# Kernel tuning notes

Hardware: AMD Instinct MI355X
Metric: run time of the kernel (lower is better)

## Reference

```python
import jax, jax.numpy as jnp
import numpy as np

NUM_HEADS = 16
NEG_INF = -9e15


def setup_inputs() -> dict:
    key = jax.random.key(0)
    k1, k2, k3 = jax.random.split(key, 3)
    B, S, D = 2, 2048, 1024
    # xavier-uniform-ish init scale for weights
    lim_qkv = float(np.sqrt(6.0 / (D + 3 * D)))
    lim_o = float(np.sqrt(6.0 / (D + D)))
    return {
        "x": jax.random.normal(k1, (B, S, D), dtype=jnp.float32),
        "w_qkv": jax.random.uniform(k2, (3 * D, D), minval=-lim_qkv, maxval=lim_qkv, dtype=jnp.float32),
        "b_qkv": jnp.zeros((3 * D,), dtype=jnp.float32),
        "w_o": jax.random.uniform(k3, (D, D), minval=-lim_o, maxval=lim_o, dtype=jnp.float32),
        "b_o": jnp.zeros((D,), dtype=jnp.float32),
    }


def reference(x, w_qkv, b_qkv, w_o, b_o):
    B, S, D = x.shape
    H = NUM_HEADS
    hd = D // H
    # qkv projection: [B,S,3D]
    qkv = x @ w_qkv.T + b_qkv
    # -> [B, H, S, 3*hd], then split
    qkv = qkv.reshape(B, S, H, 3 * hd).transpose(0, 2, 1, 3)
    q, k, v = jnp.split(qkv, 3, axis=-1)  # each [B,H,S,hd]
    scale = 1.0 / jnp.sqrt(jnp.asarray(hd, dtype=x.dtype))
    logits = jnp.einsum("bhqd,bhkd->bhqk", q, k) * scale
    attn = jax.nn.softmax(logits, axis=-1)
    vals = jnp.einsum("bhqk,bhkd->bhqd", attn, v)
    vals = vals.transpose(0, 2, 1, 3).reshape(B, S, D)
    return vals @ w_o.T + b_o
```

## Files before the change

kernel.cpp:

```cpp
#include <hip/hip_runtime.h>
#include <math.h>

#define NHEADS 16
#define HD 64

typedef __attribute__((ext_vector_type(8))) _Float16 half8;
typedef __attribute__((ext_vector_type(4))) _Float16 half4;
typedef __attribute__((ext_vector_type(4))) float f32x4;
typedef __attribute__((ext_vector_type(16))) float f32x16;
typedef __attribute__((ext_vector_type(4))) unsigned int u32x4;

__device__ inline void load_lds16(const void* g, void* l) {
    __builtin_amdgcn_global_load_lds(
        (const __attribute__((address_space(1))) unsigned int*)g,
        (__attribute__((address_space(3))) unsigned int*)l, 16, 0, 0);
}
__device__ inline void pl32swap(unsigned int& x, unsigned int& y) {
    asm volatile("v_permlane32_swap_b32 %0, %1" : "+v"(x), "+v"(y));
}

#define NX  4194304
#define NWQ 3145728
#define NWO 1048576
__global__ void cvt_all(const float* __restrict__ x, const float* __restrict__ wq,
                        const float* __restrict__ wo, _Float16* __restrict__ xf,
                        _Float16* __restrict__ wqf, _Float16* __restrict__ wof) {
    int i = (blockIdx.x * blockDim.x + threadIdx.x) * 8;
    const float* src; _Float16* dst; int off;
    if (i < NX)            { src = x;  dst = xf;  off = i; }
    else if (i < NX + NWQ) { src = wq; dst = wqf; off = i - NX; }
    else                   { src = wo; dst = wof; off = i - (NX + NWQ); }
    float4 a = *(const float4*)(src + off);
    float4 b = *(const float4*)(src + off + 4);
    half8 h;
    h[0] = (_Float16)a.x; h[1] = (_Float16)a.y; h[2] = (_Float16)a.z; h[3] = (_Float16)a.w;
    h[4] = (_Float16)b.x; h[5] = (_Float16)b.y; h[6] = (_Float16)b.z; h[7] = (_Float16)b.w;
    *(half8*)(dst + off) = h;
}

#define GEMM_SETUP(K, NTILE)                                                           \
    const int tid = threadIdx.x;                                                       \
    const int l = tid & 63, w = tid >> 6;                                              \
    const int wr = w >> 1, wc = w & 1;                                                 \
    const int nwg = gridDim.x * gridDim.y;                                             \
    const int bid = blockIdx.y * gridDim.x + blockIdx.x;                               \
    const int swz = (bid & 7) * (nwg >> 3) + (bid >> 3);                               \
    const int m0 = (swz / gridDim.x) * 128, n0 = (swz % gridDim.x) * (NTILE);          \
    const int srow = tid >> 2;                                                         \
    const int schunk = (tid & 3) ^ ((srow >> 1) & 3);                                  \
    const size_t gA0 = (size_t)(m0 + srow) * K + schunk * 8;                           \
    const size_t gA1 = gA0 + (size_t)64 * K;                                           \
    const size_t gB0 = (size_t)(n0 + srow) * K + schunk * 8;                           \
    unsigned char* ldsW = smem + w * 1024;                                             \
    const int col16 = l & 15, kc = l >> 4;                                             \
    const int ra0 = wr * 64 + col16;                                                   \
    const int offA = ra0 * 64 + ((kc ^ ((ra0 >> 1) & 3)) * 16);

#define QSCALE 0.18033688f
__global__ __launch_bounds__(256, 2) void gemm_qkv(
    const _Float16* __restrict__ A, const _Float16* __restrict__ B,
    const float* __restrict__ bias,
    _Float16* __restrict__ Qf, _Float16* __restrict__ Kf,
    _Float16* __restrict__ VfT, int K) {
    __shared__ __align__(1024) unsigned char smem[49152];
    GEMM_SETUP(K, 128)
    const size_t gB1 = gB0 + (size_t)64 * K;
    const int rb0 = wc * 64 + col16;
    const int offB = rb0 * 64 + ((kc ^ ((rb0 >> 1) & 3)) * 16);
    f32x4 acc[4][4] = {};

#define GSTAGE(k0_, buf_)                                                              \
    load_lds16(A + gA0 + (k0_), ldsW + (buf_) * 16384 + 0);                            \
    load_lds16(A + gA1 + (k0_), ldsW + (buf_) * 16384 + 4096);                         \
    load_lds16(B + gB0 + (k0_), ldsW + (buf_) * 16384 + 8192);                         \
    load_lds16(B + gB1 + (k0_), ldsW + (buf_) * 16384 + 12288);
#define GSTEP(s_, buf_, VM, dostage)                                                   \
    asm volatile("s_waitcnt " VM ::: "memory");                                        \
    __builtin_amdgcn_sched_barrier(0);                                                 \
    __builtin_amdgcn_s_barrier();                                                      \
    if (dostage) { GSTAGE(((s_) + 2) * 32, ((buf_) + 2) % 3) }                         \
    {                                                                                  \
        const unsigned char* bs = smem + (buf_) * 16384;                               \
        half8 af[4], bf[4];                                                            \
        _Pragma("unroll")                                                              \
        for (int m = 0; m < 4; ++m) af[m] = *(const half8*)(bs + offA + m * 1024);     \
        _Pragma("unroll")                                                              \
        for (int n = 0; n < 4; ++n) bf[n] = *(const half8*)(bs + 8192 + offB + n * 1024); \
        _Pragma("unroll")                                                              \
        for (int m = 0; m < 4; ++m)                                                    \
            _Pragma("unroll")                                                          \
            for (int n = 0; n < 4; ++n)                                                \
                acc[m][n] = __builtin_amdgcn_mfma_f32_16x16x32_f16(af[m], bf[n], acc[m][n], 0, 0, 0); \
    }

    GSTAGE(0, 0)
    GSTAGE(32, 1)
    for (int t = 0; t < 30; t += 3) {
        GSTEP(t, 0, "vmcnt(4)", 1)
        GSTEP(t + 1, 1, "vmcnt(4)", 1)
        GSTEP(t + 2, 2, "vmcnt(4)", 1)
    }
    GSTEP(30, 0, "vmcnt(4)", 0)
    GSTEP(31, 1, "vmcnt(0)", 0)
#undef GSTAGE
#undef GSTEP

    const int rowb = m0 + wr * 64 + (l >> 4) * 4;
    const int colb = n0 + wc * 64 + col16;
    #pragma unroll
    for (int n = 0; n < 4; ++n) {
        int col = colb + n * 16;
        int h = col / 192;
        int rem = col - h * 192;
        int part = rem >> 6, d = rem & 63;
        float bv = bias[col];
        #pragma unroll
        for (int m = 0; m < 4; ++m) {
            int r0 = rowb + m * 16;
            int b = r0 >> 11, s0r = r0 & 2047;
            int bh = b * 16 + h;
            if (part == 0) {
                #pragma unroll
                for (int j = 0; j < 4; ++j)
                    Qf[((size_t)bh * 2048 + s0r + j) * 64 + d] =
                        (_Float16)((acc[m][n][j] + bv) * QSCALE);
            } else if (part == 1) {
                #pragma unroll
                for (int j = 0; j < 4; ++j)
                    Kf[((size_t)bh * 2048 + s0r + j) * 64 + d] = (_Float16)(acc[m][n][j] + bv);
            } else {
                half4 pk;
                pk[0] = (_Float16)(acc[m][n][0] + bv);
                pk[1] = (_Float16)(acc[m][n][1] + bv);
                pk[2] = (_Float16)(acc[m][n][2] + bv);
                pk[3] = (_Float16)(acc[m][n][3] + bv);
                *(half4*)&VfT[((size_t)bh * 64 + d) * 2048 + s0r] = pk;
            }
        }
    }
}

__global__ __launch_bounds__(256, 2) void gemm_o(
    const _Float16* __restrict__ A, const _Float16* __restrict__ B,
    const float* __restrict__ bias, float* __restrict__ C,
    int M, int N, int K) {
    __shared__ __align__(1024) unsigned char smem[36864];
    GEMM_SETUP(K, 64)
    const int rb0 = wc * 32 + col16;
    const int offB = rb0 * 64 + ((kc ^ ((rb0 >> 1) & 3)) * 16);
    f32x4 acc[4][2] = {};

#define OSTAGE(k0_, buf_)                                                              \
    load_lds16(A + gA0 + (k0_), ldsW + (buf_) * 12288 + 0);                            \
    load_lds16(A + gA1 + (k0_), ldsW + (buf_) * 12288 + 4096);                         \
    load_lds16(B + gB0 + (k0_), ldsW + (buf_) * 12288 + 8192);
#define OSTEP(s_, buf_, VM, dostage)                                                   \
    asm volatile("s_waitcnt " VM ::: "memory");                                        \
    __builtin_amdgcn_sched_barrier(0);                                                 \
    __builtin_amdgcn_s_barrier();                                                      \
    if (dostage) { OSTAGE(((s_) + 2) * 32, ((buf_) + 2) % 3) }                         \
    {                                                                                  \
        const unsigned char* bs = smem + (buf_) * 12288;                               \
        half8 af[4], bf[2];                                                            \
        _Pragma("unroll")                                                              \
        for (int m = 0; m < 4; ++m) af[m] = *(const half8*)(bs + offA + m * 1024);     \
        _Pragma("unroll")                                                              \
        for (int n = 0; n < 2; ++n) bf[n] = *(const half8*)(bs + 8192 + offB + n * 1024); \
        _Pragma("unroll")                                                              \
        for (int m = 0; m < 4; ++m)                                                    \
            _Pragma("unroll")                                                          \
            for (int n = 0; n < 2; ++n)                                                \
                acc[m][n] = __builtin_amdgcn_mfma_f32_16x16x32_f16(af[m], bf[n], acc[m][n], 0, 0, 0); \
    }

    OSTAGE(0, 0)
    OSTAGE(32, 1)
    for (int t = 0; t < 30; t += 3) {
        OSTEP(t, 0, "vmcnt(3)", 1)
        OSTEP(t + 1, 1, "vmcnt(3)", 1)
        OSTEP(t + 2, 2, "vmcnt(3)", 1)
    }
    OSTEP(30, 0, "vmcnt(3)", 0)
    OSTEP(31, 1, "vmcnt(0)", 0)
#undef OSTAGE
#undef OSTEP

    const int rowb = m0 + wr * 64 + (l >> 4) * 4;
    const int colb = n0 + wc * 32 + col16;
    float bv[2];
    #pragma unroll
    for (int n = 0; n < 2; ++n) bv[n] = bias[colb + n * 16];
    #pragma unroll
    for (int m = 0; m < 4; ++m)
        #pragma unroll
        for (int j = 0; j < 4; ++j) {
            float* crow = C + (size_t)(rowb + m * 16 + j) * N + colb;
            #pragma unroll
            for (int n = 0; n < 2; ++n) crow[n * 16] = acc[m][n][j] + bv[n];
        }
}

__global__ __launch_bounds__(512, 2) void mfma_attn(
    const _Float16* __restrict__ Qf, const _Float16* __restrict__ Kf,
    const _Float16* __restrict__ VfT, _Float16* __restrict__ vals) {
    __shared__ __align__(1024) unsigned char smem[49152];
    const int tid = threadIdx.x;
    const int l = tid & 63, w = tid >> 6;
    const int l31 = l & 31, hl = l >> 5;
    const int hwbid = blockIdx.y * gridDim.x + blockIdx.x;
    const int q_t = (hwbid >> 3) & 7;
    const int bh = (hwbid & 7) + ((hwbid >> 6) << 3);
    const int q0 = q_t * 256;
    const int h = bh & 15, b = bh >> 4;

    half8 qf[4];
    {
        const _Float16* qp = Qf + ((size_t)bh * 2048 + q0 + w * 32 + l31) * 64 + hl * 8;
        #pragma unroll
        for (int c = 0; c < 4; ++c) qf[c] = *(const half8*)(qp + c * 16);
    }
    f32x16 zvec = {};
    f32x16 o0 = {}, o1 = {};
    float mshift = 0.f, lsum = 0.f;

    const _Float16* Kg = Kf + (size_t)bh * 2048 * 64;
    const _Float16* Vg = VfT + (size_t)bh * 64 * 2048;

    int offK, offV;
    {
        int row2 = w * 4 + (l >> 4);
        int slot = (l & 15) ^ (row2 & 15);
        int row = row2 * 2 + (slot >> 3);
        int chunk = slot & 7;
        offK = row * 64 + chunk * 8;
        offV = row * 2048 + chunk * 8;
    }
    const int sbase = (l31 & 1) * 8;
    const int xr = (l31 >> 1) & 15;
    const int rb0 = (l31 >> 1) * 256;

    #define STAGE(kt0, buf)                                                            \
        {                                                                              \
            unsigned char* bK = smem + (buf) * 8192 + w * 1024;                        \
            unsigned char* bV = smem + 24576 + (buf) * 8192 + w * 1024;                \
            load_lds16(Kg + (size_t)(kt0) * 64 + offK, bK);                            \
            load_lds16(Vg + (kt0) + offV, bV);                                         \
        }

    #define QK_TILE(kb, D0, D1)                                                        \
        {                                                                              \
            const unsigned char* Ksb_ = smem + (kb) * 8192;                            \
            {                                                                          \
                int chOff = ((sbase + hl) ^ xr) << 4;                                  \
                half8 k0_ = *(const half8*)(Ksb_ + rb0 + chOff);                       \
                half8 k1_ = *(const half8*)(Ksb_ + rb0 + 4096 + chOff);                \
                D0 = __builtin_amdgcn_mfma_f32_32x32x16_f16(k0_, qf[0], zvec, 0, 0, 0);\
                D1 = __builtin_amdgcn_mfma_f32_32x32x16_f16(k1_, qf[0], zvec, 0, 0, 0);\
            }                                                                          \
            _Pragma("unroll")                                                          \
            for (int kc = 1; kc < 4; ++kc) {                                           \
                int chOff = ((sbase + kc * 2 + hl) ^ xr) << 4;                         \
                half8 k0_ = *(const half8*)(Ksb_ + rb0 + chOff);                       \
                half8 k1_ = *(const half8*)(Ksb_ + rb0 + 4096 + chOff);                \
                D0 = __builtin_amdgcn_mfma_f32_32x32x16_f16(k0_, qf[kc], D0, 0, 0, 0); \
                D1 = __builtin_amdgcn_mfma_f32_32x32x16_f16(k1_, qf[kc], D1, 0, 0, 0); \
            }                                                                          \
        }

    #define SMPV(S0, S1, vb_)                                                          \
        {                                                                              \
            const unsigned char* Vsb_ = smem + 24576 + (vb_) * 8192;                   \
            if (__any(mshift != 0.f)) {                                                \
                _Pragma("unroll")                                                      \
                for (int r = 0; r < 16; ++r) { S0[r] -= mshift; S1[r] -= mshift; }     \
            }                                                                          \
            float r0 = 0.f, r1 = 0.f, r2 = 0.f, r3 = 0.f;                              \
            unsigned int a[2][8];                                                      \
            _Pragma("unroll")                                                          \
            for (int j = 0; j < 8; ++j) {                                              \
                float p0 = __builtin_amdgcn_exp2f(S0[2 * j]);                          \
                float p1 = __builtin_amdgcn_exp2f(S0[2 * j + 1]);                      \
                float q0_ = __builtin_amdgcn_exp2f(S1[2 * j]);                         \
                float q1_ = __builtin_amdgcn_exp2f(S1[2 * j + 1]);                     \
                r0 += p0; r1 += p1; r2 += q0_; r3 += q1_;                              \
                a[0][j] = __builtin_bit_cast(unsigned int, __builtin_amdgcn_cvt_pkrtz(p0, p1));   \
                a[1][j] = __builtin_bit_cast(unsigned int, __builtin_amdgcn_cvt_pkrtz(q0_, q1_)); \
            }                                                                          \
            float rsum = (r0 + r1) + (r2 + r3);                                        \
            if (__any(rsum > 32768.f)) {                                               \
                float pmax = S0[0];                                                    \
                _Pragma("unroll")                                                      \
                for (int r = 1; r < 16; ++r) pmax = fmaxf(pmax, S0[r]);                \
                _Pragma("unroll")                                                      \
                for (int r = 0; r < 16; ++r) pmax = fmaxf(pmax, S1[r]);                \
                pmax = fmaxf(pmax, __shfl_xor(pmax, 32, 64));                          \
                float d_ = fmaxf(pmax, 0.f);                                           \
                float corr = __builtin_amdgcn_exp2f(-d_);                              \
                _Pragma("unroll")                                                      \
                for (int r = 0; r < 16; ++r) { S0[r] -= d_; S1[r] -= d_; }             \
                _Pragma("unroll")                                                      \
                for (int r = 0; r < 16; ++r) { o0[r] *= corr; o1[r] *= corr; }         \
                lsum *= corr;                                                          \
                mshift += d_;                                                          \
                r0 = r1 = r2 = r3 = 0.f;                                               \
                _Pragma("unroll")                                                      \
                for (int j = 0; j < 8; ++j) {                                          \
                    float p0 = __builtin_amdgcn_exp2f(S0[2 * j]);                      \
                    float p1 = __builtin_amdgcn_exp2f(S0[2 * j + 1]);                  \
                    float q0_ = __builtin_amdgcn_exp2f(S1[2 * j]);                     \
                    float q1_ = __builtin_amdgcn_exp2f(S1[2 * j + 1]);                 \
                    r0 += p0; r1 += p1; r2 += q0_; r3 += q1_;                          \
                    a[0][j] = __builtin_bit_cast(unsigned int, __builtin_amdgcn_cvt_pkrtz(p0, p1));   \
                    a[1][j] = __builtin_bit_cast(unsigned int, __builtin_amdgcn_cvt_pkrtz(q0_, q1_)); \
                }                                                                      \
                rsum = (r0 + r1) + (r2 + r3);                                          \
            }                                                                          \
            lsum += rsum;                                                              \
            _Pragma("unroll")                                                          \
            for (int c = 0; c < 2; ++c) {                                              \
                pl32swap(a[c][0], a[c][2]);                                            \
                pl32swap(a[c][1], a[c][3]);                                            \
                pl32swap(a[c][4], a[c][6]);                                            \
                pl32swap(a[c][5], a[c][7]);                                            \
            }                                                                          \
            _Pragma("unroll")                                                          \
            for (int kk = 0; kk < 4; ++kk) {                                           \
                u32x4 pw;                                                              \
                pw.x = a[kk >> 1][(kk & 1) * 4 + 0];                                   \
                pw.y = a[kk >> 1][(kk & 1) * 4 + 1];                                   \
                pw.z = a[kk >> 1][(kk & 1) * 4 + 2];                                   \
                pw.w = a[kk >> 1][(kk & 1) * 4 + 3];                                   \
                half8 pf = __builtin_bit_cast(half8, pw);                              \
                int chOff = ((sbase + kk * 2 + hl) ^ xr) << 4;                         \
                half8 v0 = *(const half8*)(Vsb_ + rb0 + chOff);                        \
                half8 v1 = *(const half8*)(Vsb_ + rb0 + 4096 + chOff);                 \
                o0 = __builtin_amdgcn_mfma_f32_32x32x16_f16(v0, pf, o0, 0, 0, 0);      \
                o1 = __builtin_amdgcn_mfma_f32_32x32x16_f16(v1, pf, o1, 0, 0, 0);      \
            }                                                                          \
        }

    #define AITER(tt, kb, VM, dostage)                                                 \
        asm volatile("s_waitcnt " VM ::: "memory");                                    \
        __builtin_amdgcn_sched_barrier(0);                                             \
        __builtin_amdgcn_s_barrier();                                                  \
        if (dostage) STAGE(((tt) + 2) * 64, ((kb) + 2) % 3)                            \
        QK_TILE(kb, sS0, sS1)                                                          \
        SMPV(sS0, sS1, kb)

    STAGE(0, 0)
    STAGE(64, 1)
    f32x16 sS0, sS1;
    for (int t = 0; t < 30; t += 3) {
        AITER(t, 0, "vmcnt(2)", 1)
        AITER(t + 1, 1, "vmcnt(2)", 1)
        AITER(t + 2, 2, "vmcnt(2)", 1)
    }
    AITER(30, 0, "vmcnt(2)", 0)
    AITER(31, 1, "vmcnt(0)", 0)

    lsum += __shfl_xor(lsum, 32, 64);
    float inv = 1.f / lsum;
    size_t orow = ((size_t)(b * 2048 + q0 + w * 32 + l31)) * 1024 + h * 64;
    #pragma unroll
    for (int dc = 0; dc < 2; ++dc) {
        const f32x16* op = dc ? &o1 : &o0;
        #pragma unroll
        for (int rq = 0; rq < 4; ++rq) {
            int d0 = dc * 32 + rq * 8 + hl * 4;
            half4 hv;
            #pragma unroll
            for (int j = 0; j < 4; ++j) hv[j] = (_Float16)((*op)[rq * 4 + j] * inv);
            *(half4*)(vals + orow + d0) = hv;
        }
    }
}

extern "C" void kernel_launch(void* const* d_in, const int* in_sizes, int n_in,
                              void* d_out, int out_size, void* d_ws, size_t ws_size,
                              hipStream_t stream) {
    const float* x     = (const float*)d_in[0];
    const float* w_qkv = (const float*)d_in[1];
    const float* b_qkv = (const float*)d_in[2];
    const float* w_o   = (const float*)d_in[3];
    const float* b_o   = (const float*)d_in[4];
    float* out = (float*)d_out;

    const int B = 2, S = 2048, D = 1024;
    const int M = B * S;
    const int N1 = 3 * D;
    const int BH = B * NHEADS;

    _Float16* xf  = (_Float16*)d_ws;
    _Float16* wqf = xf  + (size_t)M * D;
    _Float16* wof = wqf + (size_t)N1 * D;
    _Float16* Qf  = wof + (size_t)D * D;
    _Float16* Kf  = Qf  + (size_t)BH * S * HD;
    _Float16* VfT = Kf  + (size_t)BH * S * HD;
    _Float16* vals = xf;

    cvt_all<<<(NX + NWQ + NWO) / 2048, 256, 0, stream>>>(x, w_qkv, w_o, xf, wqf, wof);

    gemm_qkv<<<dim3(N1 / 128, M / 128), 256, 0, stream>>>(xf, wqf, b_qkv, Qf, Kf, VfT, D);

    mfma_attn<<<dim3(S / 256, BH), 512, 0, stream>>>(Qf, Kf, VfT, vals);

    gemm_o<<<dim3(D / 64, M / 128), 256, 0, stream>>>(vals, wof, b_o, out, M, D, D);
}
```

Before: 107.2 us.

## Process KV tiles in pairs per barrier with doubled LDS ring

The attention loop now stages and consumes two 64-key K/V tiles per iteration. This halves the number of s_barrier/waitcnt synchronisation points and gives the scheduler two independent QK MFMA chains to interleave. LDS usage doubles to 96 KB per block, which with 512-thread blocks and launch_bounds(512,2) may reduce how many blocks fit per CU. It also raises register pressure from the extra score accumulators.

```diff
diff --git a/kernel.cpp b/kernel.cpp
--- a/kernel.cpp
+++ b/kernel.cpp
@@ -203,7 +203,7 @@
 __global__ __launch_bounds__(512, 2) void mfma_attn(
     const _Float16* __restrict__ Qf, const _Float16* __restrict__ Kf,
     const _Float16* __restrict__ VfT, _Float16* __restrict__ vals) {
-    __shared__ __align__(1024) unsigned char smem[49152];
+    __shared__ __align__(1024) unsigned char smem[98304];
     const int tid = threadIdx.x;
     const int l = tid & 63, w = tid >> 6;
     const int l31 = l & 31, hl = l >> 5;
@@ -239,17 +239,21 @@
     const int xr = (l31 >> 1) & 15;
     const int rb0 = (l31 >> 1) * 256;
 
-    #define STAGE(kt0, buf)                                                            \
+    #define STAGE_PAIR(p_)                                                             \
         {                                                                              \
-            unsigned char* bK = smem + (buf) * 8192 + w * 1024;                        \
-            unsigned char* bV = smem + 24576 + (buf) * 8192 + w * 1024;                \
-            load_lds16(Kg + (size_t)(kt0) * 64 + offK, bK);                            \
-            load_lds16(Vg + (kt0) + offV, bV);                                         \
-        }
-
-    #define QK_TILE(kb, D0, D1)                                                        \
+            int kt0_ = (p_) * 128;                                                     \
+            int s0_ = 2 * ((p_) % 3);                                                  \
+            unsigned char* bK0 = smem + s0_ * 8192 + w * 1024;                         \
+            unsigned char* bV0 = smem + 49152 + s0_ * 8192 + w * 1024;                 \
+            load_lds16(Kg + (size_t)kt0_ * 64 + offK, bK0);                            \
+            load_lds16(Vg + kt0_ + offV, bV0);                                         \
+            load_lds16(Kg + (size_t)(kt0_ + 64) * 64 + offK, bK0 + 8192);              \
+            load_lds16(Vg + (kt0_ + 64) + offV, bV0 + 8192);                           \
+        }
+
+    #define QK_TILE(slot_, D0, D1)                                                     \
         {                                                                              \
-            const unsigned char* Ksb_ = smem + (kb) * 8192;                            \
+            const unsigned char* Ksb_ = smem + (slot_) * 8192;                         \
             {                                                                          \
                 int chOff = ((sbase + hl) ^ xr) << 4;                                  \
                 half8 k0_ = *(const half8*)(Ksb_ + rb0 + chOff);                       \
@@ -267,9 +271,9 @@
             }                                                                          \
         }
 
-    #define SMPV(S0, S1, vb_)                                                          \
+    #define SMPV(S0, S1, slot_)                                                        \
         {                                                                              \
-            const unsigned char* Vsb_ = smem + 24576 + (vb_) * 8192;                   \
+            const unsigned char* Vsb_ = smem + 49152 + (slot_) * 8192;                 \
             if (__any(mshift != 0.f)) {                                                \
                 _Pragma("unroll")                                                      \
                 for (int r = 0; r < 16; ++r) { S0[r] -= mshift; S1[r] -= mshift; }     \
@@ -339,24 +343,28 @@
             }                                                                          \
         }
 
-    #define AITER(tt, kb, VM, dostage)                                                 \
+    #define PITER(p_, sl_, VM, dostage)                                                \
         asm volatile("s_waitcnt " VM ::: "memory");                                    \
         __builtin_amdgcn_sched_barrier(0);                                             \
         __builtin_amdgcn_s_barrier();                                                  \
-        if (dostage) STAGE(((tt) + 2) * 64, ((kb) + 2) % 3)                            \
-        QK_TILE(kb, sS0, sS1)                                                          \
-        SMPV(sS0, sS1, kb)
-
-    STAGE(0, 0)
-    STAGE(64, 1)
-    f32x16 sS0, sS1;
-    for (int t = 0; t < 30; t += 3) {
-        AITER(t, 0, "vmcnt(2)", 1)
-        AITER(t + 1, 1, "vmcnt(2)", 1)
-        AITER(t + 2, 2, "vmcnt(2)", 1)
-    }
-    AITER(30, 0, "vmcnt(2)", 0)
-    AITER(31, 1, "vmcnt(0)", 0)
+        if (dostage) STAGE_PAIR((p_) + 2)                                              \
+        QK_TILE(2 * (sl_), sA0, sA1)                                                   \
+        QK_TILE(2 * (sl_) + 1, sB0, sB1)                                               \
+        SMPV(sA0, sA1, 2 * (sl_))                                                      \
+        SMPV(sB0, sB1, 2 * (sl_) + 1)
+
+    STAGE_PAIR(0)
+    STAGE_PAIR(1)
+    f32x16 sA0, sA1, sB0, sB1;
+    for (int p = 0; p < 12; p += 3) {
+        PITER(p, 0, "vmcnt(4)", 1)
+        PITER(p + 1, 1, "vmcnt(4)", 1)
+        PITER(p + 2, 2, "vmcnt(4)", 1)
+    }
+    PITER(12, 0, "vmcnt(4)", 1)
+    PITER(13, 1, "vmcnt(4)", 1)
+    PITER(14, 2, "vmcnt(4)", 0)
+    PITER(15, 0, "vmcnt(0)", 0)
 
     lsum += __shfl_xor(lsum, 32, 64);
     float inv = 1.f / lsum;
```

After: 106.8 us. Within noise of the previous version (-0.4%).

## Load K/V tiles directly into registers instead of staging through LDS

Applied to the files above, without the earlier changes.

Removes the shared-memory triple-buffered staging of K and V tiles, along with the per-iteration barriers. Each wave now loads its own K and V fragments straight from global memory into registers, double-buffered for K. This removes LDS traffic and block-wide synchronization. In exchange, the 8 waves that share a head no longer share one copy of K/V, so global/L2 traffic grows about 8x, register pressure rises, and latency hiding depends on the compiler's scheduling.

```diff
diff --git a/kernel.cpp b/kernel.cpp
--- a/kernel.cpp
+++ b/kernel.cpp
@@ -203,7 +203,6 @@
 __global__ __launch_bounds__(512, 2) void mfma_attn(
     const _Float16* __restrict__ Qf, const _Float16* __restrict__ Kf,
     const _Float16* __restrict__ VfT, _Float16* __restrict__ vals) {
-    __shared__ __align__(1024) unsigned char smem[49152];
     const int tid = threadIdx.x;
     const int l = tid & 63, w = tid >> 6;
     const int l31 = l & 31, hl = l >> 5;
@@ -223,53 +222,41 @@
     f32x16 o0 = {}, o1 = {};
     float mshift = 0.f, lsum = 0.f;
 
-    const _Float16* Kg = Kf + (size_t)bh * 2048 * 64;
-    const _Float16* Vg = VfT + (size_t)bh * 64 * 2048;
-
-    int offK, offV;
-    {
-        int row2 = w * 4 + (l >> 4);
-        int slot = (l & 15) ^ (row2 & 15);
-        int row = row2 * 2 + (slot >> 3);
-        int chunk = slot & 7;
-        offK = row * 64 + chunk * 8;
-        offV = row * 2048 + chunk * 8;
-    }
-    const int sbase = (l31 & 1) * 8;
-    const int xr = (l31 >> 1) & 15;
-    const int rb0 = (l31 >> 1) * 256;
-
-    #define STAGE(kt0, buf)                                                            \
+    const _Float16* kp = Kf + (size_t)bh * 2048 * 64 + (size_t)l31 * 64 + hl * 8;
+    const _Float16* vp = VfT + (size_t)bh * 64 * 2048 + (size_t)l31 * 2048 + hl * 8;
+
+    #define LOADK(buf, kt0)                                                            \
         {                                                                              \
-            unsigned char* bK = smem + (buf) * 8192 + w * 1024;                        \
-            unsigned char* bV = smem + 24576 + (buf) * 8192 + w * 1024;                \
-            load_lds16(Kg + (size_t)(kt0) * 64 + offK, bK);                            \
-            load_lds16(Vg + (kt0) + offV, bV);                                         \
-        }
-
-    #define QK_TILE(kb, D0, D1)                                                        \
+            const _Float16* kp_ = kp + (size_t)(kt0) * 64;                             \
+            _Pragma("unroll")                                                          \
+            for (int kc = 0; kc < 4; ++kc) {                                           \
+                buf[kc * 2 + 0] = *(const half8*)(kp_ + kc * 16);                      \
+                buf[kc * 2 + 1] = *(const half8*)(kp_ + 2048 + kc * 16);               \
+            }                                                                          \
+        }
+    #define LOADV(buf, kt0)                                                            \
         {                                                                              \
-            const unsigned char* Ksb_ = smem + (kb) * 8192;                            \
-            {                                                                          \
-                int chOff = ((sbase + hl) ^ xr) << 4;                                  \
-                half8 k0_ = *(const half8*)(Ksb_ + rb0 + chOff);                       \
-                half8 k1_ = *(const half8*)(Ksb_ + rb0 + 4096 + chOff);                \
-                D0 = __builtin_amdgcn_mfma_f32_32x32x16_f16(k0_, qf[0], zvec, 0, 0, 0);\
-                D1 = __builtin_amdgcn_mfma_f32_32x32x16_f16(k1_, qf[0], zvec, 0, 0, 0);\
-            }                                                                          \
+            const _Float16* vp_ = vp + (kt0);                                          \
+            _Pragma("unroll")                                                          \
+            for (int kk = 0; kk < 4; ++kk) {                                           \
+                buf[kk * 2 + 0] = *(const half8*)(vp_ + kk * 16);                      \
+                buf[kk * 2 + 1] = *(const half8*)(vp_ + 65536 + kk * 16);              \
+            }                                                                          \
+        }
+
+    #define QK_R(kb, D0, D1)                                                           \
+        {                                                                              \
+            D0 = __builtin_amdgcn_mfma_f32_32x32x16_f16(kb[0], qf[0], zvec, 0, 0, 0);  \
+            D1 = __builtin_amdgcn_mfma_f32_32x32x16_f16(kb[1], qf[0], zvec, 0, 0, 0);  \
             _Pragma("unroll")                                                          \
             for (int kc = 1; kc < 4; ++kc) {                                           \
-                int chOff = ((sbase + kc * 2 + hl) ^ xr) << 4;                         \
-                half8 k0_ = *(const half8*)(Ksb_ + rb0 + chOff);                       \
-                half8 k1_ = *(const half8*)(Ksb_ + rb0 + 4096 + chOff);                \
-                D0 = __builtin_amdgcn_mfma_f32_32x32x16_f16(k0_, qf[kc], D0, 0, 0, 0); \
-                D1 = __builtin_amdgcn_mfma_f32_32x32x16_f16(k1_, qf[kc], D1, 0, 0, 0); \
-            }                                                                          \
-        }
-
-    #define SMPV(S0, S1, vb_)                                                          \
+                D0 = __builtin_amdgcn_mfma_f32_32x32x16_f16(kb[kc * 2 + 0], qf[kc], D0, 0, 0, 0); \
+                D1 = __builtin_amdgcn_mfma_f32_32x32x16_f16(kb[kc * 2 + 1], qf[kc], D1, 0, 0, 0); \
+            }                                                                          \
+        }
+
+    #define SMPV_R(S0, S1, vb)                                                         \
         {                                                                              \
-            const unsigned char* Vsb_ = smem + 24576 + (vb_) * 8192;                   \
             if (__any(mshift != 0.f)) {                                                \
                 _Pragma("unroll")                                                      \
                 for (int r = 0; r < 16; ++r) { S0[r] -= mshift; S1[r] -= mshift; }     \
@@ -331,32 +318,24 @@
                 pw.z = a[kk >> 1][(kk & 1) * 4 + 2];                                   \
                 pw.w = a[kk >> 1][(kk & 1) * 4 + 3];                                   \
                 half8 pf = __builtin_bit_cast(half8, pw);                              \
-                int chOff = ((sbase + kk * 2 + hl) ^ xr) << 4;                         \
-                half8 v0 = *(const half8*)(Vsb_ + rb0 + chOff);                        \
-                half8 v1 = *(const half8*)(Vsb_ + rb0 + 4096 + chOff);                 \
-                o0 = __builtin_amdgcn_mfma_f32_32x32x16_f16(v0, pf, o0, 0, 0, 0);      \
-                o1 = __builtin_amdgcn_mfma_f32_32x32x16_f16(v1, pf, o1, 0, 0, 0);      \
-            }                                                                          \
-        }
-
-    #define AITER(tt, kb, VM, dostage)                                                 \
-        asm volatile("s_waitcnt " VM ::: "memory");                                    \
-        __builtin_amdgcn_sched_barrier(0);                                             \
-        __builtin_amdgcn_s_barrier();                                                  \
-        if (dostage) STAGE(((tt) + 2) * 64, ((kb) + 2) % 3)                            \
-        QK_TILE(kb, sS0, sS1)                                                          \
-        SMPV(sS0, sS1, kb)
-
-    STAGE(0, 0)
-    STAGE(64, 1)
+                o0 = __builtin_amdgcn_mfma_f32_32x32x16_f16(vb[kk * 2 + 0], pf, o0, 0, 0, 0); \
+                o1 = __builtin_amdgcn_mfma_f32_32x32x16_f16(vb[kk * 2 + 1], pf, o1, 0, 0, 0); \
+            }                                                                          \
+        }
+
+    half8 kA[8], kB[8], vv[8];
     f32x16 sS0, sS1;
-    for (int t = 0; t < 30; t += 3) {
-        AITER(t, 0, "vmcnt(2)", 1)
-        AITER(t + 1, 1, "vmcnt(2)", 1)
-        AITER(t + 2, 2, "vmcnt(2)", 1)
-    }
-    AITER(30, 0, "vmcnt(2)", 0)
-    AITER(31, 1, "vmcnt(0)", 0)
+    LOADK(kA, 0)
+    for (int t = 0; t < 32; t += 2) {
+        LOADV(vv, t * 64)
+        if (t + 1 < 32) LOADK(kB, (t + 1) * 64)
+        QK_R(kA, sS0, sS1)
+        SMPV_R(sS0, sS1, vv)
+        LOADV(vv, (t + 1) * 64)
+        if (t + 2 < 32) LOADK(kA, (t + 2) * 64)
+        QK_R(kB, sS0, sS1)
+        SMPV_R(sS0, sS1, vv)
+    }
 
     lsum += __shfl_xor(lsum, 32, 64);
     float inv = 1.f / lsum;
```

Result: slower. 179.8 us (+67.6%).

## Halve attention block size to 128 queries with 4 waves, doubling grid

Applied to the files above, without the earlier changes.

The attention kernel now uses 256-thread blocks, each covering 128 query rows, launched as a 1D grid of 512 blocks instead of 256 blocks of 512 threads. Each wave now stages two 16-byte chunks each of K and V per tile, so the vmcnt waits move from 2 to 4. K and V for a pipeline slot are interleaved in one 16 KB region, and the block-index swizzle is redone for the new grid. The aim is more blocks for better CU load balance and occupancy, at the cost of each K/V tile being reused across fewer query rows, which raises global and L2 traffic.

```diff
diff --git a/kernel.cpp b/kernel.cpp
--- a/kernel.cpp
+++ b/kernel.cpp
@@ -200,17 +200,19 @@
         }
 }
 
-__global__ __launch_bounds__(512, 2) void mfma_attn(
+__global__ __launch_bounds__(256, 2) void mfma_attn(
     const _Float16* __restrict__ Qf, const _Float16* __restrict__ Kf,
     const _Float16* __restrict__ VfT, _Float16* __restrict__ vals) {
     __shared__ __align__(1024) unsigned char smem[49152];
     const int tid = threadIdx.x;
     const int l = tid & 63, w = tid >> 6;
     const int l31 = l & 31, hl = l >> 5;
-    const int hwbid = blockIdx.y * gridDim.x + blockIdx.x;
-    const int q_t = (hwbid >> 3) & 7;
-    const int bh = (hwbid & 7) + ((hwbid >> 6) << 3);
-    const int q0 = q_t * 256;
+    const int hwbid = blockIdx.x;
+    const int r_ = hwbid & 7;
+    const int q_t = (hwbid >> 3) & 15;
+    const int g_ = hwbid >> 7;
+    const int bh = r_ + 8 * g_;
+    const int q0 = q_t * 128;
     const int h = bh & 15, b = bh >> 4;
 
     half8 qf[4];
@@ -226,14 +228,15 @@
     const _Float16* Kg = Kf + (size_t)bh * 2048 * 64;
     const _Float16* Vg = VfT + (size_t)bh * 64 * 2048;
 
-    int offK, offV;
-    {
-        int row2 = w * 4 + (l >> 4);
+    int offK[2], offV[2];
+    #pragma unroll
+    for (int i = 0; i < 2; ++i) {
+        int row2 = w * 8 + i * 4 + (l >> 4);
         int slot = (l & 15) ^ (row2 & 15);
         int row = row2 * 2 + (slot >> 3);
         int chunk = slot & 7;
-        offK = row * 64 + chunk * 8;
-        offV = row * 2048 + chunk * 8;
+        offK[i] = row * 64 + chunk * 8;
+        offV[i] = row * 2048 + chunk * 8;
     }
     const int sbase = (l31 & 1) * 8;
     const int xr = (l31 >> 1) & 15;
@@ -241,15 +244,17 @@
 
     #define STAGE(kt0, buf)                                                            \
         {                                                                              \
-            unsigned char* bK = smem + (buf) * 8192 + w * 1024;                        \
-            unsigned char* bV = smem + 24576 + (buf) * 8192 + w * 1024;                \
-            load_lds16(Kg + (size_t)(kt0) * 64 + offK, bK);                            \
-            load_lds16(Vg + (kt0) + offV, bV);                                         \
-        }
-
-    #define QK_TILE(kb, D0, D1)                                                        \
+            unsigned char* bK = smem + (buf) * 16384 + w * 2048;                       \
+            unsigned char* bV = bK + 8192;                                             \
+            load_lds16(Kg + (size_t)(kt0) * 64 + offK[0], bK);                         \
+            load_lds16(Kg + (size_t)(kt0) * 64 + offK[1], bK + 1024);                  \
+            load_lds16(Vg + (kt0) + offV[0], bV);                                      \
+            load_lds16(Vg + (kt0) + offV[1], bV + 1024);                               \
+        }
+
+    #define QK_TILE(slot_, D0, D1)                                                     \
         {                                                                              \
-            const unsigned char* Ksb_ = smem + (kb) * 8192;                            \
+            const unsigned char* Ksb_ = smem + (slot_) * 16384;                        \
             {                                                                          \
                 int chOff = ((sbase + hl) ^ xr) << 4;                                  \
                 half8 k0_ = *(const half8*)(Ksb_ + rb0 + chOff);                       \
@@ -267,9 +272,9 @@
             }                                                                          \
         }
 
-    #define SMPV(S0, S1, vb_)                                                          \
+    #define SMPV(S0, S1, slot_)                                                        \
         {                                                                              \
-            const unsigned char* Vsb_ = smem + 24576 + (vb_) * 8192;                   \
+            const unsigned char* Vsb_ = smem + (slot_) * 16384 + 8192;                 \
             if (__any(mshift != 0.f)) {                                                \
                 _Pragma("unroll")                                                      \
                 for (int r = 0; r < 16; ++r) { S0[r] -= mshift; S1[r] -= mshift; }     \
@@ -351,11 +356,11 @@
     STAGE(64, 1)
     f32x16 sS0, sS1;
     for (int t = 0; t < 30; t += 3) {
-        AITER(t, 0, "vmcnt(2)", 1)
-        AITER(t + 1, 1, "vmcnt(2)", 1)
-        AITER(t + 2, 2, "vmcnt(2)", 1)
-    }
-    AITER(30, 0, "vmcnt(2)", 0)
+        AITER(t, 0, "vmcnt(4)", 1)
+        AITER(t + 1, 1, "vmcnt(4)", 1)
+        AITER(t + 2, 2, "vmcnt(4)", 1)
+    }
+    AITER(30, 0, "vmcnt(4)", 0)
     AITER(31, 1, "vmcnt(0)", 0)
 
     lsum += __shfl_xor(lsum, 32, 64);
@@ -402,7 +407,7 @@
 
     gemm_qkv<<<dim3(N1 / 128, M / 128), 256, 0, stream>>>(xf, wqf, b_qkv, Qf, Kf, VfT, D);
 
-    mfma_attn<<<dim3(S / 256, BH), 512, 0, stream>>>(Qf, Kf, VfT, vals);
+    mfma_attn<<<dim3(512), 256, 0, stream>>>(Qf, Kf, VfT, vals);
 
     gemm_o<<<dim3(D / 64, M / 128), 256, 0, stream>>>(vals, wof, b_o, out, M, D, D);
 }
```

Result: slower. 109.8 us (+2.4%).
